# Optimization experiments

Hardware: AMD Instinct MI355X
Metric: run time of the kernel (lower is better)

The kernel has to match this reference:

```python
import jax, jax.numpy as jnp
import numpy as np

N_NODES = 100000
N_EDGES = 1600000
N_GRAPHS = 512


def gcn_conv(x, src, dst, W, b, n_nodes):
    """PyG GCNConv: add self-loops, symmetric norm, linear, scatter-add, bias."""
    h = x @ W.T                                   # [N, out]
    ones = jnp.ones(src.shape[0], dtype=x.dtype)
    deg = jax.ops.segment_sum(ones, dst, num_segments=n_nodes)   # in-degree incl. self-loops
    dinv = jnp.where(deg > 0, jax.lax.rsqrt(deg), 0.0)
    norm = dinv[src] * dinv[dst]                  # [E+N]
    msg = h[src] * norm[:, None]                  # gather + scale
    out = jax.ops.segment_sum(msg, dst, num_segments=n_nodes)
    return out + b


def setup_inputs() -> dict:
    key = jax.random.key(0)
    ks = jax.random.split(key, 8)
    x = jax.random.normal(ks[0], (N_NODES, 2), dtype=jnp.float32)
    edge_index = jax.random.randint(ks[1], (2, N_EDGES), 0, N_NODES, dtype=jnp.int64)
    batch = jnp.sort(jax.random.randint(ks[2], (N_NODES,), 0, N_GRAPHS, dtype=jnp.int64))
    def glorot(k, shape):
        lim = jnp.sqrt(6.0 / (shape[0] + shape[1])).astype(jnp.float32)
        return jax.random.uniform(k, shape, jnp.float32, -lim, lim)
    return {
        "x": x, "edge_index": edge_index, "batch": batch,
        "W1": glorot(ks[3], (32, 2)),  "b1": jnp.zeros(32, jnp.float32),
        "W2": glorot(ks[4], (64, 32)), "b2": jnp.zeros(64, jnp.float32),
        "W3": glorot(ks[5], (32, 64)), "b3": jnp.zeros(32, jnp.float32),
        "Wfc": glorot(ks[6], (1, 32)), "bfc": jnp.zeros(1, jnp.float32),
    }


def reference(x, edge_index, batch, W1, b1, W2, b2, W3, b3, Wfc, bfc):
    n = x.shape[0]
    loop = jnp.arange(n, dtype=edge_index.dtype)
    src = jnp.concatenate([edge_index[0], loop])  # self-loops appended once
    dst = jnp.concatenate([edge_index[1], loop])

    h = jax.nn.relu(gcn_conv(x, src, dst, W1, b1, n))   # dropout = identity (eval)
    h = jax.nn.relu(gcn_conv(h, src, dst, W2, b2, n))
    h = jax.nn.relu(gcn_conv(h, src, dst, W3, b3, n))

    # global_mean_pool over graph ids
    sums = jax.ops.segment_sum(h, batch, num_segments=N_GRAPHS)
    cnts = jax.ops.segment_sum(jnp.ones((n,), h.dtype), batch, num_segments=N_GRAPHS)
    pooled = sums / jnp.maximum(cnts, 1.0)[:, None]     # [G, 32]
    return pooled @ Wfc.T + bfc                         # [G, 1]
```

## Files before the change

kernel.cpp:

```cpp
#include <hip/hip_runtime.h>
#include <hip/hip_fp16.h>


static constexpr int TPB = 256;
static constexpr int NB1 = 256;
static constexpr int NB_SCAN = 256;
static constexpr int P2CAP = 6144;

__global__ void p1_hist_kernel(const int* __restrict__ dst, int* __restrict__ hist,
                               int E, int chunk, int shift, int B) {
  __shared__ int h[1024];
  int b = blockIdx.x, t = threadIdx.x;
  for (int i = t; i < B; i += TPB) h[i] = 0;
  __syncthreads();
  int lo = b * chunk, hi = min(lo + chunk, E);
  for (int e = lo + t; e < hi; e += TPB) atomicAdd(&h[dst[e] >> shift], 1);
  __syncthreads();
  for (int i = t; i < B; i += TPB) hist[i * NB1 + b] = h[i];
}

__global__ void scan_partial_kernel(const int* __restrict__ a, int* __restrict__ bsum,
                                    int n, int seg) {
  int b = blockIdx.x, t = threadIdx.x;
  int lo = b * seg, hi = min(lo + seg, n);
  int acc = 0;
  for (int i = lo + t; i < hi; i += TPB) acc += a[i];
  __shared__ int red[TPB];
  red[t] = acc;
  __syncthreads();
  for (int st = TPB / 2; st > 0; st >>= 1) {
    if (t < st) red[t] += red[t + st];
    __syncthreads();
  }
  if (t == 0) bsum[b] = red[0];
}

__global__ void scan_blocks_kernel(int* __restrict__ bsum) {
  __shared__ int cs[NB_SCAN];
  int t = threadIdx.x;
  int v = bsum[t];
  cs[t] = v;
  __syncthreads();
  for (int off = 1; off < NB_SCAN; off <<= 1) {
    int u = (t >= off) ? cs[t - off] : 0;
    __syncthreads();
    cs[t] += u;
    __syncthreads();
  }
  bsum[t] = cs[t] - v;
}

__global__ void scan_emit_kernel(int* __restrict__ a, const int* __restrict__ bsum,
                                 int n, int seg) {
  int b = blockIdx.x, t = threadIdx.x;
  int lo = b * seg, hi = min(lo + seg, n);
  __shared__ int cs[TPB];
  __shared__ int s_run;
  if (t == 0) s_run = bsum[b];
  __syncthreads();
  for (int base = lo; base < hi; base += TPB) {
    int i = base + t;
    int v = (i < hi) ? a[i] : 0;
    cs[t] = v;
    __syncthreads();
    for (int off = 1; off < TPB; off <<= 1) {
      int u = (t >= off) ? cs[t - off] : 0;
      __syncthreads();
      cs[t] += u;
      __syncthreads();
    }
    if (i < hi) a[i] = s_run + cs[t] - v;
    __syncthreads();
    if (t == 0) s_run += cs[TPB - 1];
    __syncthreads();
  }
}

__global__ void p1_scatter_kernel(const int* __restrict__ src, const int* __restrict__ dst,
                                  const int* __restrict__ hist, unsigned int* __restrict__ epk,
                                  int E, int chunk, int shift, int srcbits, int B) {
  __shared__ int cur[1024];
  int b = blockIdx.x, t = threadIdx.x;
  for (int i = t; i < B; i += TPB) cur[i] = hist[i * NB1 + b];
  __syncthreads();
  int lo = b * chunk, hi = min(lo + chunk, E);
  int span1 = (1 << shift) - 1;
  for (int e = lo + t; e < hi; e += TPB) {
    int d = dst[e];
    int pos = atomicAdd(&cur[d >> shift], 1);
    epk[pos] = ((unsigned int)(d & span1) << srcbits) | (unsigned int)src[e];
  }
}

__global__ __launch_bounds__(TPB) void p2_sort_kernel(
    const unsigned int* __restrict__ epk, const int* __restrict__ hist,
    int* __restrict__ rowptr, float* __restrict__ dinv, int* __restrict__ esrc,
    int N, int E, int shift, int srcbits, int B) {
  int bkt = blockIdx.x, t = threadIdx.x;
  int span = 1 << shift;
  unsigned int smask = (1u << srcbits) - 1u;
  int nb = bkt << shift;
  int bstart = hist[bkt * NB1];
  int bend = (bkt + 1 < B) ? hist[(bkt + 1) * NB1] : E;
  int bsize = bend - bstart;
  __shared__ int cnt[256];
  __shared__ int ex[256];
  __shared__ int lsrc[P2CAP];
  if (t < span) cnt[t] = 0;
  __syncthreads();
  for (int e = bstart + t; e < bend; e += TPB) atomicAdd(&cnt[epk[e] >> srcbits], 1);
  __syncthreads();
  int v = (t < span) ? cnt[t] : 0;
  ex[t] = v;
  __syncthreads();
  for (int off = 1; off < 256; off <<= 1) {
    int u = (t >= off) ? ex[t - off] : 0;
    __syncthreads();
    ex[t] += u;
    __syncthreads();
  }
  int excl = ex[t] - v;
  int node = nb + t;
  if (t < span && node < N) {
    rowptr[node] = bstart + excl;
    dinv[node] = rsqrtf((float)v + 1.0f);
  }
  if (bkt == 0 && t == 0) rowptr[N] = E;
  __syncthreads();
  bool stage = (bsize <= P2CAP);
  if (t < span) cnt[t] = stage ? excl : bstart + excl;
  __syncthreads();
  for (int e = bstart + t; e < bend; e += TPB) {
    unsigned int p = epk[e];
    int pos = atomicAdd(&cnt[p >> srcbits], 1);
    if (stage) lsrc[pos] = (int)(p & smask);
    else esrc[pos] = (int)(p & smask);
  }
  __syncthreads();
  if (stage)
    for (int i = t; i < bsize; i += TPB) esrc[bstart + i] = lsrc[i];
}

__global__ void gptr_kernel(const int* __restrict__ batch, int* __restrict__ gstart, int n, int G) {
  int i = blockIdx.x * blockDim.x + threadIdx.x;
  if (i >= n) return;
  int b = batch[i];
  int bp = (i == 0) ? -1 : batch[i - 1];
  for (int g = bp + 1; g <= b; ++g) gstart[g] = i;
  if (i == n - 1)
    for (int g = b + 1; g <= G; ++g) gstart[g] = n;
}

__global__ void u0_kernel(const float2* __restrict__ x2, const float* __restrict__ dinv,
                          float2* __restrict__ u0, int n) {
  int i = blockIdx.x * blockDim.x + threadIdx.x;
  if (i >= n) return;
  float2 v = x2[i];
  float d = dinv[i];
  u0[i] = make_float2(v.x * d, v.y * d);
}

__global__ void gather2_kernel(const float2* __restrict__ u0, const int* __restrict__ rowptr,
                               const int* __restrict__ esrc, float2* __restrict__ U0, int n) {
  int i = blockIdx.x * blockDim.x + threadIdx.x;
  if (i >= n) return;
  float2 acc = u0[i];
  int r0 = rowptr[i], r1 = rowptr[i + 1];
  for (int e = r0; e < r1; ++e) {
    float2 v = u0[esrc[e]];
    acc.x += v.x;
    acc.y += v.y;
  }
  U0[i] = acc;
}

__global__ void transform1b_kernel(const float2* __restrict__ U0, const float* __restrict__ W1,
                                   const float* __restrict__ b1, const float* __restrict__ dinv,
                                   float* __restrict__ u1_32, __half* __restrict__ u1_16, int n) {
  int tid = blockIdx.x * blockDim.x + threadIdx.x;
  int i = tid >> 5, f = tid & 31;
  if (i >= n) return;
  float2 U = U0[i];
  float di = dinv[i];
  float h = fmaxf(di * (W1[f * 2 + 0] * U.x + W1[f * 2 + 1] * U.y) + b1[f], 0.f);
  float uv = di * h;
  u1_32[(size_t)i * 32 + f] = uv;
  u1_16[(size_t)i * 32 + f] = __float2half(uv);
}

template <bool EPI>
__global__ void gather32_kernel(const float4* __restrict__ a32, const float4* __restrict__ a16,
                                const int* __restrict__ rowptr, const int* __restrict__ esrc,
                                const float* __restrict__ dinv, const float* __restrict__ b,
                                float4* __restrict__ out4, int n) {
  int tid = blockIdx.x * blockDim.x + threadIdx.x;
  int i = tid >> 2, q = tid & 3;
  if (i >= n) return;
  float acc[8];
  float4 s0 = a32[(size_t)i * 8 + 2 * q];
  float4 s1 = a32[(size_t)i * 8 + 2 * q + 1];
  acc[0] = s0.x; acc[1] = s0.y; acc[2] = s0.z; acc[3] = s0.w;
  acc[4] = s1.x; acc[5] = s1.y; acc[6] = s1.z; acc[7] = s1.w;
  int r0 = rowptr[i], r1 = rowptr[i + 1];
  for (int e = r0; e < r1; ++e) {
    int s = esrc[e];
    union { float4 f4; __half2 h2[4]; } u;
    u.f4 = a16[(size_t)s * 4 + q];
    float2 a0 = __half22float2(u.h2[0]);
    float2 a1 = __half22float2(u.h2[1]);
    float2 a2 = __half22float2(u.h2[2]);
    float2 a3 = __half22float2(u.h2[3]);
    acc[0] += a0.x; acc[1] += a0.y; acc[2] += a1.x; acc[3] += a1.y;
    acc[4] += a2.x; acc[5] += a2.y; acc[6] += a3.x; acc[7] += a3.y;
  }
  float4 o0, o1;
  if (EPI) {
    float di = dinv[i];
    const float4 bv0 = ((const float4*)b)[2 * q];
    const float4 bv1 = ((const float4*)b)[2 * q + 1];
    o0.x = fmaxf(di * acc[0] + bv0.x, 0.f);
    o0.y = fmaxf(di * acc[1] + bv0.y, 0.f);
    o0.z = fmaxf(di * acc[2] + bv0.z, 0.f);
    o0.w = fmaxf(di * acc[3] + bv0.w, 0.f);
    o1.x = fmaxf(di * acc[4] + bv1.x, 0.f);
    o1.y = fmaxf(di * acc[5] + bv1.y, 0.f);
    o1.z = fmaxf(di * acc[6] + bv1.z, 0.f);
    o1.w = fmaxf(di * acc[7] + bv1.w, 0.f);
  } else {
    o0 = make_float4(acc[0], acc[1], acc[2], acc[3]);
    o1 = make_float4(acc[4], acc[5], acc[6], acc[7]);
  }
  out4[(size_t)i * 8 + 2 * q] = o0;
  out4[(size_t)i * 8 + 2 * q + 1] = o1;
}

__global__ __launch_bounds__(TPB) void t2t3_kernel(
    const float* __restrict__ U1, const float* __restrict__ W2, const float* __restrict__ b2,
    const float* __restrict__ W3, const float* __restrict__ dinv,
    float* __restrict__ g3_32, __half* __restrict__ g3_16, int n) {
  constexpr int SN = 136;
  __shared__ float U1l[32 * SN];
  __shared__ float h2l[64 * SN];
  __shared__ float W2l[32 * 68];
  __shared__ float W3l[64 * 36];
  __shared__ float dil[128];
  int t = threadIdx.x;
  int base = blockIdx.x * 128;
  for (int idx = t; idx < 2048; idx += TPB) {
    int k = idx >> 5, j = idx & 31;
    W2l[j * 68 + k] = W2[idx];
  }
  for (int idx = t; idx < 2048; idx += TPB) {
    int k = idx >> 6, j = idx & 63;
    W3l[j * 36 + k] = W3[idx];
  }
  if (t < 128) dil[t] = (base + t < n) ? dinv[base + t] : 0.f;
  for (int it = 0; it < 4; ++it) {
    int idx = it * 256 + t;
    int nl = idx >> 3, j0 = (idx & 7) * 4;
    int node = base + nl;
    float4 v = (node < n) ? ((const float4*)U1)[(size_t)node * 8 + (idx & 7)]
                          : make_float4(0.f, 0.f, 0.f, 0.f);
    U1l[(j0 + 0) * SN + nl] = v.x;
    U1l[(j0 + 1) * SN + nl] = v.y;
    U1l[(j0 + 2) * SN + nl] = v.z;
    U1l[(j0 + 3) * SN + nl] = v.w;
  }
  __syncthreads();
  {
    int a = t & 15, bb = t >> 4;
    int n0 = a * 8, k0 = bb * 4;
    float acc[4][8];
#pragma unroll
    for (int kk = 0; kk < 4; ++kk)
#pragma unroll
      for (int nn = 0; nn < 8; ++nn) acc[kk][nn] = 0.f;
#pragma unroll 8
    for (int j = 0; j < 32; ++j) {
      float4 ua = *(const float4*)&U1l[j * SN + n0];
      float4 ub = *(const float4*)&U1l[j * SN + n0 + 4];
      float4 w = *(const float4*)&W2l[j * 68 + k0];
      float un[8] = {ua.x, ua.y, ua.z, ua.w, ub.x, ub.y, ub.z, ub.w};
      float wk[4] = {w.x, w.y, w.z, w.w};
#pragma unroll
      for (int kk = 0; kk < 4; ++kk)
#pragma unroll
        for (int nn = 0; nn < 8; ++nn) acc[kk][nn] += un[nn] * wk[kk];
    }
    float4 bv = ((const float4*)b2)[bb];
    float bk[4] = {bv.x, bv.y, bv.z, bv.w};
#pragma unroll
    for (int kk = 0; kk < 4; ++kk) {
      float o[8];
#pragma unroll
      for (int nn = 0; nn < 8; ++nn)
        o[nn] = fmaxf(dil[n0 + nn] * acc[kk][nn] + bk[kk], 0.f);
      *(float4*)&h2l[(k0 + kk) * SN + n0] = make_float4(o[0], o[1], o[2], o[3]);
      *(float4*)&h2l[(k0 + kk) * SN + n0 + 4] = make_float4(o[4], o[5], o[6], o[7]);
    }
  }
  __syncthreads();
  {
    int a = t & 15, bb = t >> 4;
    int n0 = a * 8, k0 = bb * 2;
    float acc[2][8];
#pragma unroll
    for (int kk = 0; kk < 2; ++kk)
#pragma unroll
      for (int nn = 0; nn < 8; ++nn) acc[kk][nn] = 0.f;
#pragma unroll 8
    for (int j = 0; j < 64; ++j) {
      float4 ua = *(const float4*)&h2l[j * SN + n0];
      float4 ub = *(const float4*)&h2l[j * SN + n0 + 4];
      float w0 = W3l[j * 36 + k0];
      float w1 = W3l[j * 36 + k0 + 1];
      float un[8] = {ua.x, ua.y, ua.z, ua.w, ub.x, ub.y, ub.z, ub.w};
#pragma unroll
      for (int nn = 0; nn < 8; ++nn) {
        acc[0][nn] += un[nn] * w0;
        acc[1][nn] += un[nn] * w1;
      }
    }
#pragma unroll
    for (int nn = 0; nn < 8; ++nn) {
      int node = base + n0 + nn;
      if (node < n) {
        float di = dil[n0 + nn];
#pragma unroll
        for (int kk = 0; kk < 2; ++kk) {
          float gv = di * acc[kk][nn];
          g3_32[(size_t)node * 32 + k0 + kk] = gv;
          g3_16[(size_t)node * 32 + k0 + kk] = __float2half(gv);
        }
      }
    }
  }
}

__global__ void poolfc_kernel(const float* __restrict__ h3, const int* __restrict__ gstart,
                              const float* __restrict__ Wfc, const float* __restrict__ bfc,
                              float* __restrict__ out) {
  int gi = blockIdx.x;
  int s = gstart[gi], e = gstart[gi + 1];
  int t = threadIdx.x;
  int nl = t >> 5, f = t & 31;
  float acc = 0.f;
  for (int i = s + nl; i < e; i += 8) acc += h3[(size_t)i * 32 + f];
  __shared__ float red[256];
  red[t] = acc;
  __syncthreads();
  for (int st = 128; st >= 32; st >>= 1) {
    if (t < st) red[t] += red[t + st];
    __syncthreads();
  }
  if (t < 32) {
    float cnt = (float)(e - s);
    float v = (red[t] / fmaxf(cnt, 1.f)) * Wfc[t];
    for (int o = 16; o; o >>= 1) v += __shfl_down(v, o, 32);
    if (t == 0) out[gi] = v + bfc[0];
  }
}

extern "C" void kernel_launch(void* const* d_in, const int* in_sizes, int n_in,
                              void* d_out, int out_size, void* d_ws, size_t ws_size,
                              hipStream_t stream) {
  const float* x     = (const float*)d_in[0];
  const int*   ei    = (const int*)d_in[1];
  const int*   batch = (const int*)d_in[2];
  const float* W1    = (const float*)d_in[3];
  const float* b1    = (const float*)d_in[4];
  const float* W2    = (const float*)d_in[5];
  const float* b2    = (const float*)d_in[6];
  const float* W3    = (const float*)d_in[7];
  const float* b3    = (const float*)d_in[8];
  const float* Wfc   = (const float*)d_in[9];
  const float* bfc   = (const float*)d_in[10];
  float* out = (float*)d_out;

  const int N = in_sizes[0] / 2;
  const int E = in_sizes[1] / 2;
  const int G = out_size;
  const int* src = ei;
  const int* dst = ei + E;

  int shift = 7;
  while ((((N + (1 << shift) - 1) >> shift)) > 1024) ++shift;
  const int B = (N + (1 << shift) - 1) >> shift;
  const int srcbits = 32 - shift;
  const int chunkE = (E + NB1 - 1) / NB1;
  const int M = B * NB1;
  const int segM = (M + NB_SCAN - 1) / NB_SCAN;

  char* ws = (char*)d_ws;
  size_t off = 0;
  auto alloc = [&](size_t bytes) -> char* {
    char* p = ws + off;
    off += (bytes + 255) & ~(size_t)255;
    return p;
  };
  float*        dinv   = (float*)alloc((size_t)N * 4);
  int*          rowptr = (int*)alloc((size_t)(N + 1) * 4);
  int*          esrc   = (int*)alloc((size_t)E * 4);
  int*          gstart = (int*)alloc((size_t)(G + 1) * 4);
  int*          hist   = (int*)alloc((size_t)M * 4);
  int*          bsum   = (int*)alloc((size_t)NB_SCAN * 4);
  unsigned int* epk    = (unsigned int*)alloc((size_t)E * 4);
  float2*       u0     = (float2*)alloc((size_t)N * 8);
  float2*       U0     = (float2*)alloc((size_t)N * 8);
  float*        u1_32  = (float*)alloc((size_t)N * 32 * 4);
  __half*       u1_16  = (__half*)alloc((size_t)N * 32 * 2);
  float*        U1     = (float*)alloc((size_t)N * 32 * 4);
  float*        g3_32  = (float*)alloc((size_t)N * 32 * 4);
  __half*       g3_16  = (__half*)alloc((size_t)N * 32 * 2);
  float*        hA     = (float*)alloc((size_t)N * 32 * 4);

  p1_hist_kernel<<<NB1, TPB, 0, stream>>>(dst, hist, E, chunkE, shift, B);
  scan_partial_kernel<<<NB_SCAN, TPB, 0, stream>>>(hist, bsum, M, segM);
  scan_blocks_kernel<<<1, NB_SCAN, 0, stream>>>(bsum);
  scan_emit_kernel<<<NB_SCAN, TPB, 0, stream>>>(hist, bsum, M, segM);
  p1_scatter_kernel<<<NB1, TPB, 0, stream>>>(src, dst, hist, epk, E, chunkE, shift, srcbits, B);
  p2_sort_kernel<<<B, TPB, 0, stream>>>(epk, hist, rowptr, dinv, esrc, N, E, shift, srcbits, B);
  gptr_kernel<<<(N + TPB - 1) / TPB, TPB, 0, stream>>>(batch, gstart, N, G);

  u0_kernel<<<(N + TPB - 1) / TPB, TPB, 0, stream>>>((const float2*)x, dinv, u0, N);
  gather2_kernel<<<(N + TPB - 1) / TPB, TPB, 0, stream>>>(u0, rowptr, esrc, U0, N);
  transform1b_kernel<<<((size_t)N * 32 + TPB - 1) / TPB, TPB, 0, stream>>>(
      U0, W1, b1, dinv, u1_32, u1_16, N);

  gather32_kernel<false><<<((size_t)N * 4 + TPB - 1) / TPB, TPB, 0, stream>>>(
      (const float4*)u1_32, (const float4*)u1_16, rowptr, esrc, dinv, b2, (float4*)U1, N);
  t2t3_kernel<<<(N + 127) / 128, TPB, 0, stream>>>(U1, W2, b2, W3, dinv, g3_32, g3_16, N);

  gather32_kernel<true><<<((size_t)N * 4 + TPB - 1) / TPB, TPB, 0, stream>>>(
      (const float4*)g3_32, (const float4*)g3_16, rowptr, esrc, dinv, b3, (float4*)hA, N);

  poolfc_kernel<<<G, 256, 0, stream>>>(hA, gstart, Wfc, bfc, out);
}
```

Measured before the change: 256.4 us.

## Split neighbor loops across lanes and fuse layer-1 kernels into sort

The gather32 kernels now split each node's edge list across 4 lane groups, giving 16 threads per node, and combine the partial sums with xor shuffles. This adds memory-level parallelism for the high-latency random gathers. The u0 scaling is folded into p2_sort_kernel, and the layer-1 gather and transform become one kernel that uses 4 lanes per node, which removes two launches and the U0 round trip. The cost is more threads that go idle on short rows, plus extra shuffle work.

```diff
diff --git a/kernel.cpp b/kernel.cpp
--- a/kernel.cpp
+++ b/kernel.cpp
@@ -94,8 +94,9 @@
 
 __global__ __launch_bounds__(TPB) void p2_sort_kernel(
     const unsigned int* __restrict__ epk, const int* __restrict__ hist,
-    int* __restrict__ rowptr, float* __restrict__ dinv, int* __restrict__ esrc,
-    int N, int E, int shift, int srcbits, int B) {
+    const float2* __restrict__ x2,
+    int* __restrict__ rowptr, float* __restrict__ dinv, float2* __restrict__ u0,
+    int* __restrict__ esrc, int N, int E, int shift, int srcbits, int B) {
   int bkt = blockIdx.x, t = threadIdx.x;
   int span = 1 << shift;
   unsigned int smask = (1u << srcbits) - 1u;
@@ -123,7 +124,10 @@
   int node = nb + t;
   if (t < span && node < N) {
     rowptr[node] = bstart + excl;
-    dinv[node] = rsqrtf((float)v + 1.0f);
+    float dv = rsqrtf((float)v + 1.0f);
+    dinv[node] = dv;
+    float2 xv = x2[node];
+    u0[node] = make_float2(xv.x * dv, xv.y * dv);
   }
   if (bkt == 0 && t == 0) rowptr[N] = E;
   __syncthreads();
@@ -151,41 +155,40 @@
     for (int g = b + 1; g <= G; ++g) gstart[g] = n;
 }
 
-__global__ void u0_kernel(const float2* __restrict__ x2, const float* __restrict__ dinv,
-                          float2* __restrict__ u0, int n) {
-  int i = blockIdx.x * blockDim.x + threadIdx.x;
+__global__ void layer1_kernel(const float2* __restrict__ u0, const int* __restrict__ rowptr,
+                              const int* __restrict__ esrc, const float* __restrict__ W1,
+                              const float* __restrict__ b1, const float* __restrict__ dinv,
+                              float* __restrict__ u1_32, __half* __restrict__ u1_16, int n) {
+  int tid = blockIdx.x * blockDim.x + threadIdx.x;
+  int i = tid >> 2, split = tid & 3;
   if (i >= n) return;
-  float2 v = x2[i];
-  float d = dinv[i];
-  u0[i] = make_float2(v.x * d, v.y * d);
-}
-
-__global__ void gather2_kernel(const float2* __restrict__ u0, const int* __restrict__ rowptr,
-                               const int* __restrict__ esrc, float2* __restrict__ U0, int n) {
-  int i = blockIdx.x * blockDim.x + threadIdx.x;
-  if (i >= n) return;
-  float2 acc = u0[i];
+  float ax = 0.f, ay = 0.f;
+  if (split == 0) {
+    float2 s = u0[i];
+    ax = s.x; ay = s.y;
+  }
   int r0 = rowptr[i], r1 = rowptr[i + 1];
-  for (int e = r0; e < r1; ++e) {
+  for (int e = r0 + split; e < r1; e += 4) {
     float2 v = u0[esrc[e]];
-    acc.x += v.x;
-    acc.y += v.y;
-  }
-  U0[i] = acc;
-}
-
-__global__ void transform1b_kernel(const float2* __restrict__ U0, const float* __restrict__ W1,
-                                   const float* __restrict__ b1, const float* __restrict__ dinv,
-                                   float* __restrict__ u1_32, __half* __restrict__ u1_16, int n) {
-  int tid = blockIdx.x * blockDim.x + threadIdx.x;
-  int i = tid >> 5, f = tid & 31;
-  if (i >= n) return;
-  float2 U = U0[i];
+    ax += v.x; ay += v.y;
+  }
+  ax += __shfl_xor(ax, 1, 64); ay += __shfl_xor(ay, 1, 64);
+  ax += __shfl_xor(ax, 2, 64); ay += __shfl_xor(ay, 2, 64);
   float di = dinv[i];
-  float h = fmaxf(di * (W1[f * 2 + 0] * U.x + W1[f * 2 + 1] * U.y) + b1[f], 0.f);
-  float uv = di * h;
-  u1_32[(size_t)i * 32 + f] = uv;
-  u1_16[(size_t)i * 32 + f] = __float2half(uv);
+  int f0 = split * 8;
+  float o[8];
+  union { float4 f4[1]; __half h[8]; } oh;
+#pragma unroll
+  for (int k = 0; k < 8; ++k) {
+    int f = f0 + k;
+    float hv = fmaxf(di * (W1[f * 2 + 0] * ax + W1[f * 2 + 1] * ay) + b1[f], 0.f);
+    float uv = di * hv;
+    o[k] = uv;
+    oh.h[k] = __float2half(uv);
+  }
+  *(float4*)&u1_32[(size_t)i * 32 + f0] = make_float4(o[0], o[1], o[2], o[3]);
+  *(float4*)&u1_32[(size_t)i * 32 + f0 + 4] = make_float4(o[4], o[5], o[6], o[7]);
+  *(float4*)&u1_16[(size_t)i * 32 + f0] = oh.f4[0];
 }
 
 template <bool EPI>
@@ -194,15 +197,19 @@
                                 const float* __restrict__ dinv, const float* __restrict__ b,
                                 float4* __restrict__ out4, int n) {
   int tid = blockIdx.x * blockDim.x + threadIdx.x;
-  int i = tid >> 2, q = tid & 3;
+  int i = tid >> 4;
+  int sub = tid & 15;
+  int split = sub >> 2, q = sub & 3;
   if (i >= n) return;
-  float acc[8];
-  float4 s0 = a32[(size_t)i * 8 + 2 * q];
-  float4 s1 = a32[(size_t)i * 8 + 2 * q + 1];
-  acc[0] = s0.x; acc[1] = s0.y; acc[2] = s0.z; acc[3] = s0.w;
-  acc[4] = s1.x; acc[5] = s1.y; acc[6] = s1.z; acc[7] = s1.w;
+  float acc[8] = {0.f, 0.f, 0.f, 0.f, 0.f, 0.f, 0.f, 0.f};
+  if (split == 0) {
+    float4 s0 = a32[(size_t)i * 8 + 2 * q];
+    float4 s1 = a32[(size_t)i * 8 + 2 * q + 1];
+    acc[0] = s0.x; acc[1] = s0.y; acc[2] = s0.z; acc[3] = s0.w;
+    acc[4] = s1.x; acc[5] = s1.y; acc[6] = s1.z; acc[7] = s1.w;
+  }
   int r0 = rowptr[i], r1 = rowptr[i + 1];
-  for (int e = r0; e < r1; ++e) {
+  for (int e = r0 + split; e < r1; e += 4) {
     int s = esrc[e];
     union { float4 f4; __half2 h2[4]; } u;
     u.f4 = a16[(size_t)s * 4 + q];
@@ -213,6 +220,11 @@
     acc[0] += a0.x; acc[1] += a0.y; acc[2] += a1.x; acc[3] += a1.y;
     acc[4] += a2.x; acc[5] += a2.y; acc[6] += a3.x; acc[7] += a3.y;
   }
+#pragma unroll
+  for (int k = 0; k < 8; ++k) acc[k] += __shfl_xor(acc[k], 4, 64);
+#pragma unroll
+  for (int k = 0; k < 8; ++k) acc[k] += __shfl_xor(acc[k], 8, 64);
+  if (split != 0) return;
   float4 o0, o1;
   if (EPI) {
     float di = dinv[i];
@@ -406,7 +418,6 @@
   int*          bsum   = (int*)alloc((size_t)NB_SCAN * 4);
   unsigned int* epk    = (unsigned int*)alloc((size_t)E * 4);
   float2*       u0     = (float2*)alloc((size_t)N * 8);
-  float2*       U0     = (float2*)alloc((size_t)N * 8);
   float*        u1_32  = (float*)alloc((size_t)N * 32 * 4);
   __half*       u1_16  = (__half*)alloc((size_t)N * 32 * 2);
   float*        U1     = (float*)alloc((size_t)N * 32 * 4);
@@ -419,19 +430,18 @@
   scan_blocks_kernel<<<1, NB_SCAN, 0, stream>>>(bsum);
   scan_emit_kernel<<<NB_SCAN, TPB, 0, stream>>>(hist, bsum, M, segM);
   p1_scatter_kernel<<<NB1, TPB, 0, stream>>>(src, dst, hist, epk, E, chunkE, shift, srcbits, B);
-  p2_sort_kernel<<<B, TPB, 0, stream>>>(epk, hist, rowptr, dinv, esrc, N, E, shift, srcbits, B);
+  p2_sort_kernel<<<B, TPB, 0, stream>>>(epk, hist, (const float2*)x, rowptr, dinv, u0, esrc,
+                                        N, E, shift, srcbits, B);
   gptr_kernel<<<(N + TPB - 1) / TPB, TPB, 0, stream>>>(batch, gstart, N, G);
 
-  u0_kernel<<<(N + TPB - 1) / TPB, TPB, 0, stream>>>((const float2*)x, dinv, u0, N);
-  gather2_kernel<<<(N + TPB - 1) / TPB, TPB, 0, stream>>>(u0, rowptr, esrc, U0, N);
-  transform1b_kernel<<<((size_t)N * 32 + TPB - 1) / TPB, TPB, 0, stream>>>(
-      U0, W1, b1, dinv, u1_32, u1_16, N);
-
-  gather32_kernel<false><<<((size_t)N * 4 + TPB - 1) / TPB, TPB, 0, stream>>>(
+  layer1_kernel<<<((size_t)N * 4 + TPB - 1) / TPB, TPB, 0, stream>>>(
+      u0, rowptr, esrc, W1, b1, dinv, u1_32, u1_16, N);
+
+  gather32_kernel<false><<<((size_t)N * 16 + TPB - 1) / TPB, TPB, 0, stream>>>(
       (const float4*)u1_32, (const float4*)u1_16, rowptr, esrc, dinv, b2, (float4*)U1, N);
   t2t3_kernel<<<(N + 127) / 128, TPB, 0, stream>>>(U1, W2, b2, W3, dinv, g3_32, g3_16, N);
 
-  gather32_kernel<true><<<((size_t)N * 4 + TPB - 1) / TPB, TPB, 0, stream>>>(
+  gather32_kernel<true><<<((size_t)N * 16 + TPB - 1) / TPB, TPB, 0, stream>>>(
       (const float4*)g3_32, (const float4*)g3_16, rowptr, esrc, dinv, b3, (float4*)hA, N);
 
   poolfc_kernel<<<G, 256, 0, stream>>>(hA, gstart, Wfc, bfc, out);
```

Measured after the change: 248.1 us. 3.2% less time.
